# Kernel optimization log

Hardware: AMD Instinct MI355X
Metric: run time of the kernel (lower is better)

## Reference

```python
import jax, jax.numpy as jnp
import numpy as np

B, N, M, D, H = 8, 4096, 1024, 1024, 16
HD = D // H  # head_dim = 64
SCALE = HD ** -0.5
EPS = 1e-6


def _ln(x, g, b):
    mu = jnp.mean(x, axis=-1, keepdims=True)
    var = jnp.mean((x - mu) ** 2, axis=-1, keepdims=True)
    return (x - mu) * jax.lax.rsqrt(var + EPS) * g + b


def setup_inputs() -> dict:
    key = jax.random.key(0)
    ks = jax.random.split(key, 10)
    s = 0.02
    return {
        "x": jax.random.normal(ks[0], (B, N, D), jnp.float32),
        "wavelet_tokens": jax.random.normal(ks[1], (B, M, D), jnp.float32),
        "ln_q_g": jnp.ones((D,), jnp.float32),
        "ln_q_b": jnp.zeros((D,), jnp.float32),
        "Wq": jax.random.normal(ks[2], (D, D), jnp.float32) * s,
        "bq": jnp.zeros((D,), jnp.float32),
        "ln_kv_g": jnp.ones((D,), jnp.float32),
        "ln_kv_b": jnp.zeros((D,), jnp.float32),
        "Wkv": jax.random.normal(ks[3], (D, 2 * D), jnp.float32) * s,
        "bkv": jnp.zeros((2 * D,), jnp.float32),
        "Wo": jax.random.normal(ks[4], (D, D), jnp.float32) * s,
        "bo": jnp.zeros((D,), jnp.float32),
        "ln_f_g": jnp.ones((D,), jnp.float32),
        "ln_f_b": jnp.zeros((D,), jnp.float32),
        "W1": jax.random.normal(ks[5], (D, 4 * D), jnp.float32) * s,
        "b1": jnp.zeros((4 * D,), jnp.float32),
        "W2": jax.random.normal(ks[6], (4 * D, D), jnp.float32) * s,
        "b2": jnp.zeros((D,), jnp.float32),
    }


def reference(x, wavelet_tokens, ln_q_g, ln_q_b, Wq, bq, ln_kv_g, ln_kv_b,
              Wkv, bkv, Wo, bo, ln_f_g, ln_f_b, W1, b1, W2, b2):
    residual = x
    q = _ln(x, ln_q_g, ln_q_b) @ Wq + bq            # [B,N,D]
    kv = _ln(wavelet_tokens, ln_kv_g, ln_kv_b) @ Wkv + bkv  # [B,M,2D]
    k, v = kv[..., :D], kv[..., D:]
    q = q.reshape(B, N, H, HD).transpose(0, 2, 1, 3)  # [B,H,N,d]
    k = k.reshape(B, M, H, HD).transpose(0, 2, 1, 3)  # [B,H,M,d]
    v = v.reshape(B, M, H, HD).transpose(0, 2, 1, 3)
    q = jax.nn.softmax(q, axis=2) * SCALE   # softmax over spatial N
    k = jax.nn.softmax(k, axis=-1)          # softmax over head_dim
    context = jnp.einsum('bhmd,bhme->bhde', k, v)   # [B,H,d,d]
    out = jnp.einsum('bhnd,bhde->bhne', q, context)  # [B,H,N,d]
    out = out.transpose(0, 2, 1, 3).reshape(B, N, D)
    out = out @ Wo + bo
    x2 = residual + out
    h = _ln(x2, ln_f_g, ln_f_b) @ W1 + b1
    h = jax.nn.silu(h) @ W2 + b2
    return x2 + h
```

## Files before the change

### kernel.cpp

```cpp
#include <hip/hip_runtime.h>
#include <stdint.h>
#include <stddef.h>

#define BB 8
#define NN 4096
#define MTOK 1024
#define DD 1024
#define HH 16
#define EPSF 1e-6f
static const float SCALE_F = 0.125f;

typedef __attribute__((ext_vector_type(4))) float f32x4;
typedef __attribute__((ext_vector_type(8))) short bf16x8;

__device__ __forceinline__ short f2bf(float f) {
  union { float f; uint32_t u; } x; x.f = f;
  uint32_t r = (x.u + 0x7fffu + ((x.u >> 16) & 1u)) >> 16;
  return (short)(uint16_t)r;
}
__device__ __forceinline__ float bf2f(short s) {
  union { uint32_t u; float f; } x; x.u = ((uint32_t)(uint16_t)s) << 16;
  return x.f;
}

#if defined(__HIP_DEVICE_COMPILE__) && __has_builtin(__builtin_amdgcn_global_load_lds)
#define USE_GLOAD_LDS 1
#else
#define USE_GLOAD_LDS 0
#endif

#define BAR() __builtin_amdgcn_s_barrier()
#define LGKM0()                                        \
  do {                                                 \
    asm volatile("s_waitcnt lgkmcnt(0)" ::: "memory"); \
    __builtin_amdgcn_sched_barrier(0);                 \
  } while (0)
#define LGKM8() asm volatile("s_waitcnt lgkmcnt(8)" ::: "memory")
#if USE_GLOAD_LDS
#define VMW6() asm volatile("s_waitcnt vmcnt(6)" ::: "memory")
#else
#define VMW6() asm volatile("s_waitcnt vmcnt(0) lgkmcnt(0)" ::: "memory")
#endif
#define VMW0() asm volatile("s_waitcnt vmcnt(0)" ::: "memory")

__device__ __forceinline__ bf16x8 ldsld(const char* p, int off) {
  return *(const bf16x8*)(p + off);
}
template <int MH>
__device__ __forceinline__ void rdA8(const char* k0, const char* k1, bf16x8 a[4][2]) {
#pragma unroll
  for (int m = 0; m < 4; ++m) {
    a[m][0] = ldsld(k0, MH * 8192 + m * 2048);
    a[m][1] = ldsld(k1, MH * 8192 + m * 2048);
  }
}
template <int NH>
__device__ __forceinline__ void rdB4(const char* k0, const char* k1, bf16x8 b[2][2]) {
#pragma unroll
  for (int n = 0; n < 2; ++n) {
    b[n][0] = ldsld(k0, NH * 16384 + n * 2048);
    b[n][1] = ldsld(k1, NH * 16384 + n * 2048);
  }
}
__device__ __forceinline__ void stgA(char* smc, int base, const short* pg,
                                     int ld, int mh, int k, int w) {
#pragma unroll
  for (int i = 0; i < 2; ++i) {
    const short* src = pg + (long)(mh * 64 + i * 128) * ld + k;
    char* dst = smc + base + i * 16384 + mh * 8192 + w * 1024;
#if USE_GLOAD_LDS
    __builtin_amdgcn_global_load_lds(
        (const __attribute__((address_space(1))) void*)src,
        (__attribute__((address_space(3))) void*)dst, 16, 0, 0);
#else
    *(bf16x8*)(dst + (int)(threadIdx.x & 63) * 16) = *(const bf16x8*)src;
#endif
  }
}
__device__ __forceinline__ void stgB(char* smc, int base, const short* pg,
                                     int ld, int h, int k, int w) {
#pragma unroll
  for (int i = 0; i < 2; ++i) {
    const short* src = pg + (long)(h * 32 + i * 128) * ld + k;
    char* dst = smc + base + h * 16384 + i * 8192 + w * 1024;
#if USE_GLOAD_LDS
    __builtin_amdgcn_global_load_lds(
        (const __attribute__((address_space(1))) void*)src,
        (__attribute__((address_space(3))) void*)dst, 16, 0, 0);
#else
    *(bf16x8*)(dst + (int)(threadIdx.x & 63) * 16) = *(const bf16x8*)src;
#endif
  }
}
template <int MH, int NH>
__device__ __forceinline__ void mq(const bf16x8 a[4][2], const bf16x8 b[2][2],
                                   f32x4 acc[8][4]) {
  __builtin_amdgcn_s_setprio(1);
#pragma unroll
  for (int m = 0; m < 4; ++m)
#pragma unroll
    for (int n = 0; n < 2; ++n) {
      f32x4 c = acc[MH * 4 + m][NH * 2 + n];
      c = __builtin_amdgcn_mfma_f32_16x16x32_bf16(a[m][0], b[n][0], c, 0, 0, 0);
      c = __builtin_amdgcn_mfma_f32_16x16x32_bf16(a[m][1], b[n][1], c, 0, 0, 0);
      acc[MH * 4 + m][NH * 2 + n] = c;
    }
  __builtin_amdgcn_s_setprio(0);
}

template <int EPI>
__global__ __launch_bounds__(512, 2) void gemm256(
    const short* __restrict__ A, const short* __restrict__ BT,
    const float* __restrict__ bias, const float* __restrict__ resid,
    void* __restrict__ outp, int N, int K, int lda, int ldb, int num_n) {
  __shared__ int4 smem4[131072 / 16];
  char* smc = (char*)smem4;
  const int t = threadIdx.x;
  const int w = t >> 6, lane = t & 63;
  const int wr = w >> 2, wc = w & 3;

  const int nwg = gridDim.x, orig = blockIdx.x;
  const int q8 = nwg >> 3, r8 = nwg & 7;
  const int xcd = orig & 7, loc = orig >> 3;
  const int wg = (xcd < r8 ? xcd * (q8 + 1) : r8 * (q8 + 1) + (xcd - r8) * q8) + loc;
  const int bm = wg / num_n, bn = wg % num_n;

  const int T = K >> 6;

  int LA = wr * 16384 + (lane & 15) * 128 + ((lane >> 4) << 4);
  LA ^= ((LA >> 7) & 7) << 4;
  int LB = wc * 4096 + (lane & 15) * 128 + ((lane >> 4) << 4);
  LB ^= ((LB >> 7) & 7) << 4;
  const char* pA0k0 = smc + LA;
  const char* pA0k1 = smc + (LA ^ 64);
  const char* pA1k0 = pA0k0 + 65536;
  const char* pA1k1 = pA0k1 + 65536;
  const char* pB0k0 = smc + 32768 + LB;
  const char* pB0k1 = smc + 32768 + (LB ^ 64);
  const char* pB1k0 = pB0k0 + 65536;
  const char* pB1k1 = pB0k1 + 65536;

  const int colswz = ((t & 7) ^ ((t >> 3) & 7)) * 8;
  const short* pAg = A + (long)(bm * 256 + (t >> 3)) * lda + colswz;
  const short* pBg =
      BT + (long)(bn * 256 + ((t >> 8) * 64 + ((t >> 3) & 31))) * ldb + colswz;

  f32x4 acc[8][4];
#pragma unroll
  for (int i = 0; i < 8; ++i)
#pragma unroll
    for (int j = 0; j < 4; ++j) acc[i][j] = (f32x4){0.f, 0.f, 0.f, 0.f};

  bf16x8 a[4][2], b0[2][2], b1[2][2];

  stgA(smc, 0, pAg, lda, 0, 0, w);
  stgB(smc, 32768, pBg, ldb, 0, 0, w);
  stgB(smc, 32768, pBg, ldb, 1, 0, w);
  stgA(smc, 0, pAg, lda, 1, 0, w);
  stgA(smc, 65536, pAg, lda, 0, 64, w);
  stgB(smc, 98304, pBg, ldb, 0, 64, w);
  stgB(smc, 98304, pBg, ldb, 1, 64, w);
  VMW6();
  BAR();

  for (int t2 = 0; t2 < T; t2 += 2) {
    const int k1 = (t2 + 1) * 64;
    const int k2 = (t2 + 2 < T ? t2 + 2 : 0) * 64;
    const int k3 = (t2 + 3 < T ? t2 + 3 : 0) * 64;
    rdA8<0>(pA0k0, pA0k1, a);
    rdB4<0>(pB0k0, pB0k1, b0);
    stgA(smc, 65536, pAg, lda, 1, k1, w);
    LGKM8();
    BAR(); LGKM0();
    mq<0, 0>(a, b0, acc);
    BAR();
    rdB4<1>(pB0k0, pB0k1, b1);
    stgA(smc, 0, pAg, lda, 0, k2, w);
    BAR(); LGKM0();
    mq<0, 1>(a, b1, acc);
    BAR();
    rdA8<1>(pA0k0, pA0k1, a);
    stgB(smc, 32768, pBg, ldb, 0, k2, w);
    BAR(); LGKM0();
    mq<1, 0>(a, b0, acc);
    BAR();
    stgB(smc, 32768, pBg, ldb, 1, k2, w);
    VMW6();
    BAR();
    mq<1, 1>(a, b1, acc);
    BAR();
    rdA8<0>(pA1k0, pA1k1, a);
    rdB4<0>(pB1k0, pB1k1, b0);
    stgA(smc, 0, pAg, lda, 1, k2, w);
    LGKM8();
    BAR(); LGKM0();
    mq<0, 0>(a, b0, acc);
    BAR();
    rdB4<1>(pB1k0, pB1k1, b1);
    stgA(smc, 65536, pAg, lda, 0, k3, w);
    BAR(); LGKM0();
    mq<0, 1>(a, b1, acc);
    BAR();
    rdA8<1>(pA1k0, pA1k1, a);
    stgB(smc, 98304, pBg, ldb, 0, k3, w);
    BAR(); LGKM0();
    mq<1, 0>(a, b0, acc);
    BAR();
    stgB(smc, 98304, pBg, ldb, 1, k3, w);
    VMW6();
    BAR();
    mq<1, 1>(a, b1, acc);
    BAR();
  }
  VMW0();

  const int r0 = bm * 256 + wr * 128 + ((lane >> 4) << 2);
  const int c0 = bn * 256 + wc * 64 + (lane & 15);
#pragma unroll
  for (int mi = 0; mi < 8; ++mi) {
#pragma unroll
    for (int ni = 0; ni < 4; ++ni) {
      const int col = c0 + ni * 16;
      const float bv = bias ? bias[col] : 0.f;
#pragma unroll
      for (int rr = 0; rr < 4; ++rr) {
        const int row = r0 + mi * 16 + rr;
        const long idx = (long)row * N + col;
        float v = acc[mi][ni][rr] + bv;
        if (EPI == 0) {
          ((float*)outp)[idx] = v;
        } else if (EPI == 1) {
          ((float*)outp)[idx] = v + resid[idx];
        } else if (EPI == 2) {
          ((short*)outp)[idx] = f2bf(v);
        } else {
          v = v / (1.f + __expf(-v));
          ((short*)outp)[idx] = f2bf(v);
        }
      }
    }
  }
}

__global__ __launch_bounds__(256) void ln_rows(const float* __restrict__ in,
                                               const float* __restrict__ g,
                                               const float* __restrict__ bta,
                                               short* __restrict__ outp) {
  const int row = blockIdx.x;
  const int t = threadIdx.x;
  const float4 v = ((const float4*)(in + (long)row * DD))[t];
  float s = v.x + v.y + v.z + v.w;
  float ss = v.x * v.x + v.y * v.y + v.z * v.z + v.w * v.w;
#pragma unroll
  for (int off = 1; off < 64; off <<= 1) {
    s += __shfl_xor(s, off);
    ss += __shfl_xor(ss, off);
  }
  __shared__ float red[8];
  const int w = t >> 6, lane = t & 63;
  if (lane == 0) { red[w] = s; red[4 + w] = ss; }
  __syncthreads();
  s = red[0] + red[1] + red[2] + red[3];
  ss = red[4] + red[5] + red[6] + red[7];
  const float mu = s * (1.f / DD);
  const float var = ss * (1.f / DD) - mu * mu;
  const float rs = rsqrtf(var + EPSF);
  const float4 gv = ((const float4*)g)[t];
  const float4 bv = ((const float4*)bta)[t];
  short4 o;
  o.x = f2bf((v.x - mu) * rs * gv.x + bv.x);
  o.y = f2bf((v.y - mu) * rs * gv.y + bv.y);
  o.z = f2bf((v.z - mu) * rs * gv.z + bv.z);
  o.w = f2bf((v.w - mu) * rs * gv.w + bv.w);
  ((short4*)(outp + (long)row * DD))[t] = o;
}

__global__ __launch_bounds__(256) void tconv(const float* __restrict__ W,
                                             short* __restrict__ WT, int K, int N) {
  __shared__ float tile[64][65];
  const int k0 = blockIdx.x * 64, n0 = blockIdx.y * 64;
  const int t = threadIdx.x;
  const int tr = t >> 6, tc = t & 63;
#pragma unroll
  for (int i = 0; i < 64; i += 4)
    tile[i + tr][tc] = W[(long)(k0 + i + tr) * N + n0 + tc];
  __syncthreads();
#pragma unroll
  for (int i = 0; i < 64; i += 4)
    WT[(long)(n0 + i + tr) * K + k0 + tc] = f2bf(tile[tc][i + tr]);
}

__global__ __launch_bounds__(256) void ctx_kernel(const short* __restrict__ kv,
                                                  float* __restrict__ ctx) {
  const int bh = blockIdx.x;
  const int b = bh >> 4, h = bh & 15;
  const int t = threadIdx.x, g = t >> 6, lane = t & 63;
  __shared__ float ksm[4][64];
  __shared__ float vsm[4][64];
  float acc[16];
#pragma unroll
  for (int j = 0; j < 16; ++j) acc[j] = 0.f;
  const int d = t & 63;
  const int e0 = (t >> 6) * 16;
  const short* base = kv + (long)b * MTOK * 2048 + h * 64;
  for (int m0 = 0; m0 < MTOK; m0 += 4) {
    const long moff = (long)(m0 + g) * 2048;
    float kval = bf2f(base[moff + lane]);
    float vval = bf2f(base[moff + 1024 + lane]);
    float mx = kval;
#pragma unroll
    for (int off = 1; off < 64; off <<= 1) mx = fmaxf(mx, __shfl_xor(mx, off));
    float e = __expf(kval - mx);
    float sm = e;
#pragma unroll
    for (int off = 1; off < 64; off <<= 1) sm += __shfl_xor(sm, off);
    ksm[g][lane] = e / sm;
    vsm[g][lane] = vval;
    __syncthreads();
#pragma unroll
    for (int mm = 0; mm < 4; ++mm) {
      const float kd = ksm[mm][d];
#pragma unroll
      for (int j = 0; j < 16; ++j) acc[j] = fmaf(kd, vsm[mm][e0 + j], acc[j]);
    }
    __syncthreads();
  }
  float* cp = ctx + ((long)bh * 64 + d) * 64 + e0;
#pragma unroll
  for (int j = 0; j < 16; ++j) cp[j] = acc[j];
}

__global__ __launch_bounds__(256) void qstat_part(const float* __restrict__ q,
                                                  float* __restrict__ pmax,
                                                  float* __restrict__ psum) {
  const int c = blockIdx.x * 256 + threadIdx.x;
  const int b = blockIdx.z, ch = blockIdx.y;
  const float* qp = q + ((long)b * NN + ch * 128) * DD + c;
  float mx = -1e30f, sm = 0.f;
  for (int r = 0; r < 128; ++r) {
    const float xv = qp[(long)r * DD];
    const float nm = fmaxf(mx, xv);
    sm = sm * __expf(mx - nm) + __expf(xv - nm);
    mx = nm;
  }
  const long idx = ((long)b * DD + c) * 32 + ch;
  pmax[idx] = mx;
  psum[idx] = sm;
}

__global__ __launch_bounds__(256) void qstat_comb(const float* __restrict__ pmax,
                                                  const float* __restrict__ psum,
                                                  float* __restrict__ cmax,
                                                  float* __restrict__ crs) {
  const int i = blockIdx.x * 256 + threadIdx.x;
  const float* pm = pmax + (long)i * 32;
  const float* ps = psum + (long)i * 32;
  float mx = -1e30f;
#pragma unroll
  for (int ch = 0; ch < 32; ++ch) mx = fmaxf(mx, pm[ch]);
  float sm = 0.f;
#pragma unroll
  for (int ch = 0; ch < 32; ++ch) sm += ps[ch] * __expf(pm[ch] - mx);
  cmax[i] = mx;
  crs[i] = SCALE_F / sm;
}

__global__ __launch_bounds__(256) void attn_apply(const float* __restrict__ q,
                                                  const float* __restrict__ ctx,
                                                  const float* __restrict__ cmax,
                                                  const float* __restrict__ crs,
                                                  short* __restrict__ outa) {
  const int b = blockIdx.z, h = blockIdx.y, n0 = blockIdx.x * 128;
  const int t = threadIdx.x, g = t >> 6, lane = t & 63;
  __shared__ float ctx_l[4096];
  __shared__ float cm[64], cs[64];
  __shared__ float qsm[4][64];
  const float* cp = ctx + (long)(b * HH + h) * 4096;
  for (int i = t; i < 4096; i += 256) ctx_l[i] = cp[i];
  if (t < 64) {
    cm[t] = cmax[(long)b * DD + h * 64 + t];
    cs[t] = crs[(long)b * DD + h * 64 + t];
  }
  __syncthreads();
  for (int i = 0; i < 32; ++i) {
    const int n = n0 + i * 4 + g;
    const long off = ((long)b * NN + n) * DD + h * 64;
    const float qv = q[off + lane];
    const float qs = __expf(qv - cm[lane]) * cs[lane];
    qsm[g][lane] = qs;
    float o = 0.f;
#pragma unroll
    for (int dd = 0; dd < 64; ++dd) o = fmaf(qsm[g][dd], ctx_l[dd * 64 + lane], o);
    outa[off + lane] = f2bf(o);
  }
}

extern "C" void kernel_launch(void* const* d_in, const int* in_sizes, int n_in,
                              void* d_out, int out_size, void* d_ws, size_t ws_size,
                              hipStream_t stream) {
  (void)in_sizes; (void)n_in; (void)out_size;
  const float* x      = (const float*)d_in[0];
  const float* wav    = (const float*)d_in[1];
  const float* ln_q_g = (const float*)d_in[2];
  const float* ln_q_b = (const float*)d_in[3];
  const float* Wq     = (const float*)d_in[4];
  const float* bq     = (const float*)d_in[5];
  const float* ln_kv_g= (const float*)d_in[6];
  const float* ln_kv_b= (const float*)d_in[7];
  const float* Wkv    = (const float*)d_in[8];
  const float* bkv    = (const float*)d_in[9];
  const float* Wo     = (const float*)d_in[10];
  const float* bo     = (const float*)d_in[11];
  const float* ln_f_g = (const float*)d_in[12];
  const float* ln_f_b = (const float*)d_in[13];
  const float* W1     = (const float*)d_in[14];
  const float* b1     = (const float*)d_in[15];
  const float* W2     = (const float*)d_in[16];
  const float* b2     = (const float*)d_in[17];
  float* outp = (float*)d_out;
  char* ws = (char*)d_ws;

  const long MR = (long)BB * NN;
  const long MKV = (long)BB * MTOK;

  size_t off = 0;
  auto bump = [&](size_t bytes) {
    size_t o = off;
    off += (bytes + 255) & ~(size_t)255;
    return o;
  };
  short* WqT  = (short*)(ws + bump((size_t)DD * DD * 2));
  short* WkvT = (short*)(ws + bump((size_t)2048 * DD * 2));
  short* WoT  = (short*)(ws + bump((size_t)DD * DD * 2));
  short* W1T  = (short*)(ws + bump((size_t)4096 * DD * 2));
  short* W2T  = (short*)(ws + bump((size_t)DD * 4096 * 2));
  float* qbuf = (float*)(ws + bump((size_t)MR * DD * 4));
  short* lnbuf= (short*)(ws + bump((size_t)MR * DD * 2));
  float* ctx  = (float*)(ws + bump((size_t)BB * HH * 64 * 64 * 4));
  float* pmax = (float*)(ws + bump((size_t)BB * DD * 32 * 4));
  float* psum = (float*)(ws + bump((size_t)BB * DD * 32 * 4));
  float* cmax = (float*)(ws + bump((size_t)BB * DD * 4));
  float* crs  = (float*)(ws + bump((size_t)BB * DD * 4));
  const size_t dyn0 = off;
  short* wvln  = (short*)(ws + dyn0);
  short* kvbuf = (short*)(ws + dyn0 + (size_t)MKV * DD * 2);
  short* oattn = (short*)(ws + dyn0);
  short* hbuf  = (short*)(ws + dyn0);

  size_t avail = ws_size > dyn0 ? ws_size - dyn0 : 0;
  int CS = 4096;
  while (CS > 256 && (size_t)MR * CS * 2 > avail) CS >>= 1;

  const int nm = (int)(MR / 256);
  const int nmkv = (int)(MKV / 256);

  tconv<<<dim3(DD / 64, DD / 64), 256, 0, stream>>>(Wq, WqT, DD, DD);
  tconv<<<dim3(DD / 64, 2048 / 64), 256, 0, stream>>>(Wkv, WkvT, DD, 2048);
  tconv<<<dim3(DD / 64, DD / 64), 256, 0, stream>>>(Wo, WoT, DD, DD);
  tconv<<<dim3(DD / 64, 4096 / 64), 256, 0, stream>>>(W1, W1T, DD, 4096);
  tconv<<<dim3(4096 / 64, DD / 64), 256, 0, stream>>>(W2, W2T, 4096, DD);

  ln_rows<<<dim3((unsigned)MR), 256, 0, stream>>>(x, ln_q_g, ln_q_b, lnbuf);
  ln_rows<<<dim3((unsigned)MKV), 256, 0, stream>>>(wav, ln_kv_g, ln_kv_b, wvln);

  gemm256<0><<<dim3((unsigned)(nm * (DD / 256))), 512, 0, stream>>>(
      lnbuf, WqT, bq, nullptr, qbuf, DD, DD, DD, DD, DD / 256);
  gemm256<2><<<dim3((unsigned)(nmkv * (2048 / 256))), 512, 0, stream>>>(
      wvln, WkvT, bkv, nullptr, kvbuf, 2048, DD, DD, DD, 2048 / 256);
  ctx_kernel<<<dim3(BB * HH), 256, 0, stream>>>(kvbuf, ctx);
  qstat_part<<<dim3(DD / 256, 32, BB), 256, 0, stream>>>(qbuf, pmax, psum);
  qstat_comb<<<dim3(BB * DD / 256), 256, 0, stream>>>(pmax, psum, cmax, crs);
  attn_apply<<<dim3(NN / 128, HH, BB), 256, 0, stream>>>(qbuf, ctx, cmax, crs, oattn);
  gemm256<1><<<dim3((unsigned)(nm * (DD / 256))), 512, 0, stream>>>(
      oattn, WoT, bo, x, qbuf, DD, DD, DD, DD, DD / 256);
  float* x2 = qbuf;
  ln_rows<<<dim3((unsigned)MR), 256, 0, stream>>>(x2, ln_f_g, ln_f_b, lnbuf);
  for (int c0 = 0; c0 < 4096; c0 += CS) {
    gemm256<3><<<dim3((unsigned)(nm * (CS / 256))), 512, 0, stream>>>(
        lnbuf, W1T + (long)c0 * DD, b1 + c0, nullptr, hbuf, CS, DD, DD, DD, CS / 256);
    gemm256<1><<<dim3((unsigned)(nm * (DD / 256))), 512, 0, stream>>>(
        hbuf, W2T + c0, (c0 == 0) ? b2 : nullptr,
        (c0 == 0) ? (const float*)x2 : (const float*)outp, outp, DD, CS, CS, 4096, DD / 256);
  }
}
```

Measured before the change: 1.293 ms.

## Make GEMM persistent over multiple tiles and store Q projection in bf16

The 256x256 GEMM kernel becomes persistent. Each workgroup loops over NT consecutive output tiles and prefetches the next tile's first K-slices during the last phase of the current tile, which hides per-tile prologue latency and launch tail effects. The grid is sized to about 256 workgroups, and launch bounds drop to one block per CU. Separately, the Q projection now writes bf16 instead of fp32, roughly halving the traffic for the later qstat and attn_apply passes at some cost in precision before the spatial softmax.

```diff
diff --git a/kernel.cpp b/kernel.cpp
--- a/kernel.cpp
+++ b/kernel.cpp
@@ -108,11 +108,60 @@
   __builtin_amdgcn_s_setprio(0);
 }
 
+#define PHASES(PA1, PB1, PA2, PB2, K1, K2, K3)                      \
+  do {                                                              \
+    rdA8<0>(pA0k0, pA0k1, a);                                       \
+    rdB4<0>(pB0k0, pB0k1, b0);                                      \
+    stgA(smc, 65536, PA1, lda, 1, K1, w);                           \
+    LGKM8();                                                        \
+    BAR(); LGKM0();                                                 \
+    mq<0, 0>(a, b0, acc);                                           \
+    BAR();                                                          \
+    rdB4<1>(pB0k0, pB0k1, b1);                                      \
+    stgA(smc, 0, PA2, lda, 0, K2, w);                               \
+    BAR(); LGKM0();                                                 \
+    mq<0, 1>(a, b1, acc);                                           \
+    BAR();                                                          \
+    rdA8<1>(pA0k0, pA0k1, a);                                       \
+    stgB(smc, 32768, PB2, ldb, 0, K2, w);                           \
+    BAR(); LGKM0();                                                 \
+    mq<1, 0>(a, b0, acc);                                           \
+    BAR();                                                          \
+    stgB(smc, 32768, PB2, ldb, 1, K2, w);                           \
+    VMW6();                                                         \
+    BAR();                                                          \
+    mq<1, 1>(a, b1, acc);                                           \
+    BAR();                                                          \
+    rdA8<0>(pA1k0, pA1k1, a);                                       \
+    rdB4<0>(pB1k0, pB1k1, b0);                                      \
+    stgA(smc, 0, PA2, lda, 1, K2, w);                               \
+    LGKM8();                                                        \
+    BAR(); LGKM0();                                                 \
+    mq<0, 0>(a, b0, acc);                                           \
+    BAR();                                                          \
+    rdB4<1>(pB1k0, pB1k1, b1);                                      \
+    stgA(smc, 65536, PA2, lda, 0, K3, w);                           \
+    BAR(); LGKM0();                                                 \
+    mq<0, 1>(a, b1, acc);                                           \
+    BAR();                                                          \
+    rdA8<1>(pA1k0, pA1k1, a);                                       \
+    stgB(smc, 98304, PB2, ldb, 0, K3, w);                           \
+    BAR(); LGKM0();                                                 \
+    mq<1, 0>(a, b0, acc);                                           \
+    BAR();                                                          \
+    stgB(smc, 98304, PB2, ldb, 1, K3, w);                           \
+    VMW6();                                                         \
+    BAR();                                                          \
+    mq<1, 1>(a, b1, acc);                                           \
+    BAR();                                                          \
+  } while (0)
+
 template <int EPI>
-__global__ __launch_bounds__(512, 2) void gemm256(
+__global__ __launch_bounds__(512, 1) void gemm256(
     const short* __restrict__ A, const short* __restrict__ BT,
     const float* __restrict__ bias, const float* __restrict__ resid,
-    void* __restrict__ outp, int N, int K, int lda, int ldb, int num_n) {
+    void* __restrict__ outp, int N, int K, int lda, int ldb, int num_n,
+    int NT) {
   __shared__ int4 smem4[131072 / 16];
   char* smc = (char*)smem4;
   const int t = threadIdx.x;
@@ -122,8 +171,9 @@
   const int nwg = gridDim.x, orig = blockIdx.x;
   const int q8 = nwg >> 3, r8 = nwg & 7;
   const int xcd = orig & 7, loc = orig >> 3;
-  const int wg = (xcd < r8 ? xcd * (q8 + 1) : r8 * (q8 + 1) + (xcd - r8) * q8) + loc;
-  const int bm = wg / num_n, bn = wg % num_n;
+  const int pb = (xcd < r8 ? xcd * (q8 + 1) : r8 * (q8 + 1) + (xcd - r8) * q8) + loc;
+  const int wg0 = pb * NT;
+  int bm = wg0 / num_n, bn = wg0 % num_n;
 
   const int T = K >> 6;
 
@@ -141,9 +191,10 @@
   const char* pB1k1 = pB0k1 + 65536;
 
   const int colswz = ((t & 7) ^ ((t >> 3) & 7)) * 8;
-  const short* pAg = A + (long)(bm * 256 + (t >> 3)) * lda + colswz;
-  const short* pBg =
-      BT + (long)(bn * 256 + ((t >> 8) * 64 + ((t >> 3) & 31))) * ldb + colswz;
+  const long thrA = (long)(t >> 3) * lda + colswz;
+  const long thrB = (long)((t >> 8) * 64 + ((t >> 3) & 31)) * ldb + colswz;
+  const short* pAg = A + (long)bm * 256 * lda + thrA;
+  const short* pBg = BT + (long)bn * 256 * ldb + thrB;
 
   f32x4 acc[8][4];
 #pragma unroll
@@ -163,83 +214,53 @@
   VMW6();
   BAR();
 
-  for (int t2 = 0; t2 < T; t2 += 2) {
-    const int k1 = (t2 + 1) * 64;
-    const int k2 = (t2 + 2 < T ? t2 + 2 : 0) * 64;
-    const int k3 = (t2 + 3 < T ? t2 + 3 : 0) * 64;
-    rdA8<0>(pA0k0, pA0k1, a);
-    rdB4<0>(pB0k0, pB0k1, b0);
-    stgA(smc, 65536, pAg, lda, 1, k1, w);
-    LGKM8();
-    BAR(); LGKM0();
-    mq<0, 0>(a, b0, acc);
-    BAR();
-    rdB4<1>(pB0k0, pB0k1, b1);
-    stgA(smc, 0, pAg, lda, 0, k2, w);
-    BAR(); LGKM0();
-    mq<0, 1>(a, b1, acc);
-    BAR();
-    rdA8<1>(pA0k0, pA0k1, a);
-    stgB(smc, 32768, pBg, ldb, 0, k2, w);
-    BAR(); LGKM0();
-    mq<1, 0>(a, b0, acc);
-    BAR();
-    stgB(smc, 32768, pBg, ldb, 1, k2, w);
-    VMW6();
-    BAR();
-    mq<1, 1>(a, b1, acc);
-    BAR();
-    rdA8<0>(pA1k0, pA1k1, a);
-    rdB4<0>(pB1k0, pB1k1, b0);
-    stgA(smc, 0, pAg, lda, 1, k2, w);
-    LGKM8();
-    BAR(); LGKM0();
-    mq<0, 0>(a, b0, acc);
-    BAR();
-    rdB4<1>(pB1k0, pB1k1, b1);
-    stgA(smc, 65536, pAg, lda, 0, k3, w);
-    BAR(); LGKM0();
-    mq<0, 1>(a, b1, acc);
-    BAR();
-    rdA8<1>(pA1k0, pA1k1, a);
-    stgB(smc, 98304, pBg, ldb, 0, k3, w);
-    BAR(); LGKM0();
-    mq<1, 0>(a, b0, acc);
-    BAR();
-    stgB(smc, 98304, pBg, ldb, 1, k3, w);
-    VMW6();
-    BAR();
-    mq<1, 1>(a, b1, acc);
-    BAR();
-  }
-  VMW0();
-
-  const int r0 = bm * 256 + wr * 128 + ((lane >> 4) << 2);
-  const int c0 = bn * 256 + wc * 64 + (lane & 15);
-#pragma unroll
-  for (int mi = 0; mi < 8; ++mi) {
-#pragma unroll
-    for (int ni = 0; ni < 4; ++ni) {
-      const int col = c0 + ni * 16;
-      const float bv = bias ? bias[col] : 0.f;
-#pragma unroll
-      for (int rr = 0; rr < 4; ++rr) {
-        const int row = r0 + mi * 16 + rr;
-        const long idx = (long)row * N + col;
-        float v = acc[mi][ni][rr] + bv;
-        if (EPI == 0) {
-          ((float*)outp)[idx] = v;
-        } else if (EPI == 1) {
-          ((float*)outp)[idx] = v + resid[idx];
-        } else if (EPI == 2) {
-          ((short*)outp)[idx] = f2bf(v);
-        } else {
-          v = v / (1.f + __expf(-v));
-          ((short*)outp)[idx] = f2bf(v);
+  for (int it = 0; it < NT; ++it) {
+    const int wgn = wg0 + (it + 1 < NT ? it + 1 : it);
+    const int bmn = wgn / num_n, bnn = wgn % num_n;
+    const short* pAn = A + (long)bmn * 256 * lda + thrA;
+    const short* pBn = BT + (long)bnn * 256 * ldb + thrB;
+    for (int t2 = 0; t2 < T - 2; t2 += 2) {
+      PHASES(pAg, pBg, pAg, pBg, (t2 + 1) * 64, (t2 + 2) * 64, (t2 + 3) * 64);
+    }
+    PHASES(pAg, pBg, pAn, pBn, (T - 1) * 64, 0, 64);
+
+    {
+      const int r0 = bm * 256 + wr * 128 + ((lane >> 4) << 2);
+      const int c0 = bn * 256 + wc * 64 + (lane & 15);
+#pragma unroll
+      for (int mi = 0; mi < 8; ++mi) {
+#pragma unroll
+        for (int ni = 0; ni < 4; ++ni) {
+          const int col = c0 + ni * 16;
+          const float bv = bias ? bias[col] : 0.f;
+#pragma unroll
+          for (int rr = 0; rr < 4; ++rr) {
+            const int row = r0 + mi * 16 + rr;
+            const long idx = (long)row * N + col;
+            float v = acc[mi][ni][rr] + bv;
+            if (EPI == 0) {
+              ((float*)outp)[idx] = v;
+            } else if (EPI == 1) {
+              ((float*)outp)[idx] = v + resid[idx];
+            } else if (EPI == 2) {
+              ((short*)outp)[idx] = f2bf(v);
+            } else {
+              v = v / (1.f + __expf(-v));
+              ((short*)outp)[idx] = f2bf(v);
+            }
+          }
         }
       }
     }
-  }
+    if (it + 1 < NT) {
+#pragma unroll
+      for (int i = 0; i < 8; ++i)
+#pragma unroll
+        for (int j = 0; j < 4; ++j) acc[i][j] = (f32x4){0.f, 0.f, 0.f, 0.f};
+    }
+    pAg = pAn; pBg = pBn; bm = bmn; bn = bnn;
+  }
+  VMW0();
 }
 
 __global__ __launch_bounds__(256) void ln_rows(const float* __restrict__ in,
@@ -330,15 +351,15 @@
   for (int j = 0; j < 16; ++j) cp[j] = acc[j];
 }
 
-__global__ __launch_bounds__(256) void qstat_part(const float* __restrict__ q,
+__global__ __launch_bounds__(256) void qstat_part(const short* __restrict__ q,
                                                   float* __restrict__ pmax,
                                                   float* __restrict__ psum) {
   const int c = blockIdx.x * 256 + threadIdx.x;
   const int b = blockIdx.z, ch = blockIdx.y;
-  const float* qp = q + ((long)b * NN + ch * 128) * DD + c;
+  const short* qp = q + ((long)b * NN + ch * 128) * DD + c;
   float mx = -1e30f, sm = 0.f;
   for (int r = 0; r < 128; ++r) {
-    const float xv = qp[(long)r * DD];
+    const float xv = bf2f(qp[(long)r * DD]);
     const float nm = fmaxf(mx, xv);
     sm = sm * __expf(mx - nm) + __expf(xv - nm);
     mx = nm;
@@ -365,7 +386,7 @@
   crs[i] = SCALE_F / sm;
 }
 
-__global__ __launch_bounds__(256) void attn_apply(const float* __restrict__ q,
+__global__ __launch_bounds__(256) void attn_apply(const short* __restrict__ q,
                                                   const float* __restrict__ ctx,
                                                   const float* __restrict__ cmax,
                                                   const float* __restrict__ crs,
@@ -385,7 +406,7 @@
   for (int i = 0; i < 32; ++i) {
     const int n = n0 + i * 4 + g;
     const long off = ((long)b * NN + n) * DD + h * 64;
-    const float qv = q[off + lane];
+    const float qv = bf2f(q[off + lane]);
     const float qs = __expf(qv - cm[lane]) * cs[lane];
     qsm[g][lane] = qs;
     float o = 0.f;
@@ -454,6 +475,13 @@
   const int nm = (int)(MR / 256);
   const int nmkv = (int)(MKV / 256);
 
+  auto pgrid = [](int nwg) {
+    int NT = nwg / 256;
+    if (NT < 1) NT = 1;
+    while (nwg % NT) --NT;
+    return NT;
+  };
+
   tconv<<<dim3(DD / 64, DD / 64), 256, 0, stream>>>(Wq, WqT, DD, DD);
   tconv<<<dim3(DD / 64, 2048 / 64), 256, 0, stream>>>(Wkv, WkvT, DD, 2048);
   tconv<<<dim3(DD / 64, DD / 64), 256, 0, stream>>>(Wo, WoT, DD, DD);
@@ -463,23 +491,41 @@
   ln_rows<<<dim3((unsigned)MR), 256, 0, stream>>>(x, ln_q_g, ln_q_b, lnbuf);
   ln_rows<<<dim3((unsigned)MKV), 256, 0, stream>>>(wav, ln_kv_g, ln_kv_b, wvln);
 
-  gemm256<0><<<dim3((unsigned)(nm * (DD / 256))), 512, 0, stream>>>(
-      lnbuf, WqT, bq, nullptr, qbuf, DD, DD, DD, DD, DD / 256);
-  gemm256<2><<<dim3((unsigned)(nmkv * (2048 / 256))), 512, 0, stream>>>(
-      wvln, WkvT, bkv, nullptr, kvbuf, 2048, DD, DD, DD, 2048 / 256);
+  {
+    int nwg = nm * (DD / 256), NT = pgrid(nwg);
+    gemm256<2><<<dim3((unsigned)(nwg / NT)), 512, 0, stream>>>(
+        lnbuf, WqT, bq, nullptr, (short*)qbuf, DD, DD, DD, DD, DD / 256, NT);
+  }
+  {
+    int nwg = nmkv * (2048 / 256), NT = pgrid(nwg);
+    gemm256<2><<<dim3((unsigned)(nwg / NT)), 512, 0, stream>>>(
+        wvln, WkvT, bkv, nullptr, kvbuf, 2048, DD, DD, DD, 2048 / 256, NT);
+  }
   ctx_kernel<<<dim3(BB * HH), 256, 0, stream>>>(kvbuf, ctx);
-  qstat_part<<<dim3(DD / 256, 32, BB), 256, 0, stream>>>(qbuf, pmax, psum);
+  qstat_part<<<dim3(DD / 256, 32, BB), 256, 0, stream>>>((const short*)qbuf, pmax, psum);
   qstat_comb<<<dim3(BB * DD / 256), 256, 0, stream>>>(pmax, psum, cmax, crs);
-  attn_apply<<<dim3(NN / 128, HH, BB), 256, 0, stream>>>(qbuf, ctx, cmax, crs, oattn);
-  gemm256<1><<<dim3((unsigned)(nm * (DD / 256))), 512, 0, stream>>>(
-      oattn, WoT, bo, x, qbuf, DD, DD, DD, DD, DD / 256);
+  attn_apply<<<dim3(NN / 128, HH, BB), 256, 0, stream>>>((const short*)qbuf, ctx,
+                                                         cmax, crs, oattn);
+  {
+    int nwg = nm * (DD / 256), NT = pgrid(nwg);
+    gemm256<1><<<dim3((unsigned)(nwg / NT)), 512, 0, stream>>>(
+        oattn, WoT, bo, x, qbuf, DD, DD, DD, DD, DD / 256, NT);
+  }
   float* x2 = qbuf;
   ln_rows<<<dim3((unsigned)MR), 256, 0, stream>>>(x2, ln_f_g, ln_f_b, lnbuf);
   for (int c0 = 0; c0 < 4096; c0 += CS) {
-    gemm256<3><<<dim3((unsigned)(nm * (CS / 256))), 512, 0, stream>>>(
-        lnbuf, W1T + (long)c0 * DD, b1 + c0, nullptr, hbuf, CS, DD, DD, DD, CS / 256);
-    gemm256<1><<<dim3((unsigned)(nm * (DD / 256))), 512, 0, stream>>>(
-        hbuf, W2T + c0, (c0 == 0) ? b2 : nullptr,
-        (c0 == 0) ? (const float*)x2 : (const float*)outp, outp, DD, CS, CS, 4096, DD / 256);
-  }
-}
+    {
+      int nwg = nm * (CS / 256), NT = pgrid(nwg);
+      gemm256<3><<<dim3((unsigned)(nwg / NT)), 512, 0, stream>>>(
+          lnbuf, W1T + (long)c0 * DD, b1 + c0, nullptr, hbuf, CS, DD, DD, DD,
+          CS / 256, NT);
+    }
+    {
+      int nwg = nm * (DD / 256), NT = pgrid(nwg);
+      gemm256<1><<<dim3((unsigned)(nwg / NT)), 512, 0, stream>>>(
+          hbuf, W2T + c0, (c0 == 0) ? b2 : nullptr,
+          (c0 == 0) ? (const float*)x2 : (const float*)outp, outp, DD, CS, CS,
+          4096, DD / 256, NT);
+    }
+  }
+}
```

Result: slower. 1.596 ms (+23.5%).
